# Kernel optimization log

Measured on AMD Instinct MI355X. Metric: run time of the kernel, lower is better.

The kernel has to match this reference:

```python
import jax, jax.numpy as jnp
import numpy as np

DIM = 512        # channels
QK = 512         # qk_dim (defaults to dim)
HEADS = 8
NWIN = 7         # windows per side
TOPK = 4
HD_QK = QK // HEADS
HD_V = DIM // HEADS


def setup_inputs() -> dict:
    key = jax.random.key(0)
    k0, k1, k2 = jax.random.split(key, 3)
    x = jax.random.normal(k0, (16, DIM, 56, 56), jnp.float32)
    w_qkv = jax.random.normal(k1, (2 * QK + DIM, DIM), jnp.float32) * 0.02
    b_qkv = jnp.zeros((2 * QK + DIM,), jnp.float32)
    w_lepe = jax.random.normal(k2, (DIM, 1, 3, 3), jnp.float32) * 0.02
    b_lepe = jnp.zeros((DIM,), jnp.float32)
    return {"x": x, "w_qkv": w_qkv, "b_qkv": b_qkv, "w_lepe": w_lepe, "b_lepe": b_lepe}


def _window(t, N, nwin, wh, ww):
    # (N, c, H, W) -> (N, p^2, w^2, c), matching 'n c (j h) (i w) -> n (j i) (h w) c'
    c = t.shape[1]
    t = t.reshape(N, c, nwin, wh, nwin, ww)
    return t.transpose(0, 2, 4, 3, 5, 1).reshape(N, nwin * nwin, wh * ww, c)


def reference(x, w_qkv, b_qkv, w_lepe, b_lepe):
    N, C, H, W = x.shape
    scale = QK ** -0.5
    wh, ww = H // NWIN, W // NWIN
    p2, w2 = NWIN * NWIN, wh * ww

    # QKVConv: 1x1 conv == per-pixel channel matmul
    qkv = jnp.einsum('nchw,oc->nohw', x, w_qkv) + b_qkv[None, :, None, None]
    q = qkv[:, :QK]          # (N, QK, H, W)
    kv = qkv[:, QK:]         # (N, QK+DIM, H, W)
    v = kv[:, QK:]           # (N, DIM, H, W)

    # lepe: depthwise 3x3 conv, stride 1 (stride_def==1 for dim=512/'small')
    lepe = jax.lax.conv_general_dilated(
        v, w_lepe, window_strides=(1, 1), padding='SAME',
        dimension_numbers=('NCHW', 'OIHW', 'NCHW'),
        feature_group_count=DIM) + b_lepe[None, :, None, None]

    q_pix = _window(q, N, NWIN, wh, ww)    # (N, p2, w2, QK)
    kv_pix = _window(kv, N, NWIN, wh, ww)  # (N, p2, w2, QK+DIM)

    # window-level routing queries/keys (detached: diff_routing=False)
    q_win = jax.lax.stop_gradient(q_pix.mean(axis=2))            # (N, p2, QK)
    k_win = jax.lax.stop_gradient(kv_pix[..., :QK].mean(axis=2))  # (N, p2, QK)

    # TopkRouting (emb is Identity since param_routing=False)
    attn_logit = jnp.einsum('npc,nmc->npm', q_win * scale, k_win)  # (N, p2, p2)
    topk_logit, r_idx = jax.lax.top_k(attn_logit, TOPK)            # (N, p2, TOPK)
    r_weight = jax.nn.softmax(topk_logit, axis=-1)                 # unused: mul_weight='none'

    # KVGather: kv_sel[n, p, t] = kv_pix[n, r_idx[n, p, t]]
    kv_sel = jax.vmap(lambda kvn, idxn: kvn[idxn])(kv_pix, r_idx)  # (N, p2, TOPK, w2, QK+DIM)

    k_sel = kv_sel[..., :QK].reshape(N, p2, TOPK * w2, HEADS, HD_QK)
    v_sel = kv_sel[..., QK:].reshape(N, p2, TOPK * w2, HEADS, HD_V)
    q_h = q_pix.reshape(N, p2, w2, HEADS, HD_QK)

    # per-window multi-head attention over gathered KV
    attn = jnp.einsum('npqhd,npkhd->nphqk', q_h * scale, k_sel)  # (N,p2,H,w2,TOPK*w2)
    attn = jax.nn.softmax(attn, axis=-1)
    out = jnp.einsum('nphqk,npkhd->npqhd', attn, v_sel)          # (N,p2,w2,HEADS,HD_V)
    out = out.reshape(N, NWIN, NWIN, wh, ww, DIM)
    out = out.transpose(0, 5, 1, 3, 2, 4).reshape(N, DIM, H, W)

    return out + lepe
```

## Files before the change

kernel.cpp:

```cpp
#include <hip/hip_runtime.h>

#define DEVI __device__ __forceinline__

typedef __attribute__((ext_vector_type(8))) short s16x8;
typedef __attribute__((ext_vector_type(4))) short s16x4;
typedef __attribute__((ext_vector_type(4))) float f32x4;

DEVI unsigned short f2b(float f) {
  union { float f; unsigned u; } v; v.f = f;
  return (unsigned short)((v.u + 0x7fffu + ((v.u >> 16) & 1u)) >> 16);
}
DEVI float b2f(unsigned short h) {
  union { unsigned u; float f; } v; v.u = ((unsigned)h) << 16;
  return v.f;
}

DEVI void gload16(const unsigned short* g, char* l) {
  __builtin_amdgcn_global_load_lds((const __attribute__((address_space(1))) void*)g,
                                   (__attribute__((address_space(3))) void*)l, 16, 0, 0);
}

__global__ __launch_bounds__(256) void k_transpose(const float* __restrict__ x,
                                                   unsigned short* __restrict__ xt,
                                                   float* __restrict__ rsum) {
  __shared__ unsigned short tile[64][68];
  __shared__ float ftile[64][65];
  const int s0 = blockIdx.x * 64, c0 = blockIdx.y * 64, n = blockIdx.z;
  const int t = threadIdx.x;
  const float* xp = x + (size_t)n * 512 * 3136;
  const int sl = t & 63;
  const int sg = s0 + sl;
#pragma unroll
  for (int pass = 0; pass < 4; ++pass) {
    const int quad = pass * 4 + (t >> 6);
    const int cc = quad * 4;
    unsigned short e[4];
#pragma unroll
    for (int jj = 0; jj < 4; ++jj) {
      float val = (sg < 3136) ? xp[(size_t)(c0 + cc + jj) * 3136 + sg] : 0.f;
      ftile[sl][cc + jj] = val;
      e[jj] = f2b(val);
    }
    s16x4 pk = {(short)e[0], (short)e[1], (short)e[2], (short)e[3]};
    *(s16x4*)(&tile[sl][cc]) = pk;
  }
  __syncthreads();
  unsigned short* xo = xt + ((size_t)n * 3200 + s0) * 512 + c0;
#pragma unroll
  for (int pass = 0; pass < 2; ++pass) {
    const int srow = pass * 32 + (t >> 3);
    const int ch = (t & 7) * 8;
    uint2 a = *(const uint2*)(&tile[srow][ch]);
    uint2 b = *(const uint2*)(&tile[srow][ch + 4]);
    uint4 val = {a.x, a.y, b.x, b.y};
    *(uint4*)(xo + (size_t)srow * 512 + ch) = val;
  }
  if (s0 < 3136) {
#pragma unroll
    for (int k = 0; k < 2; ++k) {
      const int idx = k * 256 + t;
      const int seg = idx >> 6, c = idx & 63;
      float s = 0.f;
#pragma unroll
      for (int e = 0; e < 8; ++e) s += ftile[seg * 8 + e][c];
      rsum[((size_t)n * 392 + (s0 >> 3) + seg) * 512 + c0 + c] = s;
    }
  }
}

__global__ __launch_bounds__(256) void k_wmean2(const float* __restrict__ rsum,
                                                float* __restrict__ xwm) {
  const int wi = blockIdx.x, n = blockIdx.y;
  const int wy = wi / 7, wx = wi % 7;
  const int t = threadIdx.x;
  float s0 = 0.f, s1 = 0.f;
#pragma unroll
  for (int dy = 0; dy < 8; ++dy) {
    const float* rp = rsum + ((size_t)n * 392 + (wy * 8 + dy) * 7 + wx) * 512;
    s0 += rp[t];
    s1 += rp[t + 256];
  }
  float* dst = xwm + ((size_t)n * 49 + wi) * 512;
  dst[t] = s0 * 0.015625f;
  dst[t + 256] = s1 * 0.015625f;
}

__global__ __launch_bounds__(256) void k_cvt_w(const float* __restrict__ w,
                                               unsigned short* __restrict__ wb) {
  const int i = (blockIdx.x * 256 + threadIdx.x) * 4;
  const float4 v = *(const float4*)(w + i);
  s16x4 pk = {(short)f2b(v.x), (short)f2b(v.y), (short)f2b(v.z), (short)f2b(v.w)};
  *(s16x4*)(wb + i) = pk;
}

__global__ __launch_bounds__(256) void k_qkv_gemm(
    const unsigned short* __restrict__ wb,
    const unsigned short* __restrict__ xt,
    const float* __restrict__ b_qkv,
    unsigned short* __restrict__ q_pix,
    unsigned short* __restrict__ k_pix,
    unsigned short* __restrict__ vwinT) {
  __shared__ char smem[34816];
  const int o0 = blockIdx.x * 128, s0 = blockIdx.y * 128, n = blockIdx.z;
  const int t = threadIdx.x;
  const int wave = t >> 6, lane = t & 63;
  const int wm = wave >> 1, wn = wave & 1;
  const int r15 = lane & 15, hi4 = lane >> 4;
  const unsigned short* Ag = wb + (size_t)o0 * 512;
  const unsigned short* Bg = xt + ((size_t)n * 3200 + s0) * 512;
  const int rch = lane >> 3;
  const int gsw = (lane & 7) ^ rch;

  f32x4 acc[4][4];
#pragma unroll
  for (int a = 0; a < 4; ++a)
#pragma unroll
    for (int b = 0; b < 4; ++b) acc[a][b] = (f32x4){0.f, 0.f, 0.f, 0.f};

  for (int kk = 0; kk < 8; ++kk) {
#pragma unroll
    for (int i = 0; i < 8; ++i) {
      const int chunk = i * 4 + wave;
      const unsigned short* base = (chunk < 16) ? Ag : Bg;
      const int row = (chunk & 15) * 8 + rch;
      gload16(base + (size_t)row * 512 + kk * 64 + gsw * 8, smem + (size_t)chunk * 1024);
    }
    __syncthreads();
    s16x8 af[2][4], bfr[2][4];
#pragma unroll
    for (int m = 0; m < 4; ++m) {
      const int ra = wm * 64 + m * 16 + r15;
      const int rb = wn * 64 + m * 16 + r15;
#pragma unroll
      for (int kb = 0; kb < 2; ++kb) {
        af[kb][m]  = *(const s16x8*)(smem + (size_t)ra * 128 + (((kb * 4 + hi4) ^ (ra & 7)) * 16));
        bfr[kb][m] = *(const s16x8*)(smem + 16384 + (size_t)rb * 128 + (((kb * 4 + hi4) ^ (rb & 7)) * 16));
      }
    }
#pragma unroll
    for (int kb = 0; kb < 2; ++kb)
#pragma unroll
      for (int m = 0; m < 4; ++m)
#pragma unroll
        for (int nf = 0; nf < 4; ++nf)
          acc[m][nf] = __builtin_amdgcn_mfma_f32_16x16x32_bf16(af[kb][m], bfr[kb][nf], acc[m][nf], 0, 0, 0);
    __syncthreads();
  }

  if (o0 >= 1024) {
    const int c0v = o0 - 1024;
    unsigned short* OT2 = (unsigned short*)smem;
#pragma unroll
    for (int m = 0; m < 4; ++m)
#pragma unroll
      for (int r = 0; r < 4; ++r) {
        const int ol = wm * 64 + m * 16 + hi4 * 4 + r;
        const float bia = b_qkv[o0 + ol];
#pragma unroll
        for (int nf = 0; nf < 4; ++nf) {
          const int sl = wn * 64 + nf * 16 + r15;
          OT2[(size_t)ol * 136 + sl] = f2b(acc[m][nf][r] + bia);
        }
      }
    __syncthreads();
#pragma unroll
    for (int i = 0; i < 8; ++i) {
      const int chunk = i * 256 + t;
      const int cl = chunk >> 4;
      const int sl = (chunk & 15) * 8;
      const int s = s0 + sl;
      if (s < 3136) {
        const uint4 val = *(const uint4*)(OT2 + (size_t)cl * 136 + sl);
        const int hh = s / 56, ww = s % 56;
        const int wdw = (hh >> 3) * 7 + (ww >> 3);
        const int key = (hh & 7) * 8;
        *(uint4*)(vwinT + (((size_t)n * 49 + wdw) * 512 + c0v + cl) * 64 + key) = val;
      }
    }
    return;
  }

  const bool isQ = (o0 < 512);
  const float sf = isQ ? 1.0f : 0.044194173824159216f;
  unsigned short* OT = (unsigned short*)smem;
#pragma unroll
  for (int m = 0; m < 4; ++m) {
    const int ol = wm * 64 + m * 16 + hi4 * 4;
    float bi_[4];
#pragma unroll
    for (int r = 0; r < 4; ++r) bi_[r] = b_qkv[o0 + ol + r];
#pragma unroll
    for (int nf = 0; nf < 4; ++nf) {
      const int sl = wn * 64 + nf * 16 + r15;
      s16x4 pk = {(short)f2b((acc[m][nf][0] + bi_[0]) * sf), (short)f2b((acc[m][nf][1] + bi_[1]) * sf),
                  (short)f2b((acc[m][nf][2] + bi_[2]) * sf), (short)f2b((acc[m][nf][3] + bi_[3]) * sf)};
      *(s16x4*)(OT + (size_t)sl * 132 + ol) = pk;
    }
  }
  __syncthreads();
#pragma unroll
  for (int pass = 0; pass < 8; ++pass) {
    const int sl = pass * 16 + (t >> 4);
    const int oh = (t & 15) * 8;
    const int s = s0 + sl;
    if (s < 3136) {
      const uint2 a = *(const uint2*)((char*)smem + (size_t)sl * 264 + oh * 2);
      const uint2 b = *(const uint2*)((char*)smem + (size_t)sl * 264 + oh * 2 + 8);
      const int hh = s / 56, ww = s % 56;
      const int wdw = (hh >> 3) * 7 + (ww >> 3);
      const int pi = (hh & 7) * 8 + (ww & 7);
      const int o = o0 + oh;
      const uint4 val = {a.x, a.y, b.x, b.y};
      if (isQ)
        *(uint4*)(q_pix + (((size_t)n * 49 + wdw) * 64 + pi) * 512 + o) = val;
      else
        *(uint4*)(k_pix + (((size_t)n * 49 + wdw) * 64 + pi) * 512 + (o - 512)) = val;
    }
  }
}

__global__ __launch_bounds__(256) void k_winproj(
    const float* __restrict__ xwm, const float* __restrict__ w_qkv,
    const float* __restrict__ b_qkv, float* __restrict__ qkw) {
  __shared__ float wss[64][65];
  __shared__ float xs[56][64];
  const int o0 = blockIdx.x * 64, n = blockIdx.y;
  const int t = threadIdx.x;
  const int ot = t & 31, pt = t >> 5;
  float acc0[7], acc1[7];
#pragma unroll
  for (int jj = 0; jj < 7; ++jj) { acc0[jj] = 0.f; acc1[jj] = 0.f; }
  for (int c0 = 0; c0 < 512; c0 += 64) {
    __syncthreads();
#pragma unroll
    for (int pass = 0; pass < 4; ++pass) {
      const int oo = (t >> 4) + pass * 16;
      const int cc = (t & 15) * 4;
      const float4 v = *(const float4*)(w_qkv + (size_t)(o0 + oo) * 512 + c0 + cc);
      wss[cc + 0][oo] = v.x; wss[cc + 1][oo] = v.y; wss[cc + 2][oo] = v.z; wss[cc + 3][oo] = v.w;
    }
#pragma unroll
    for (int i = 0; i < 14; ++i) {
      const int idx = i * 256 + t;
      const int p = idx >> 6, cc = idx & 63;
      xs[p][cc] = (p < 49) ? xwm[((size_t)n * 49 + p) * 512 + c0 + cc] : 0.f;
    }
    __syncthreads();
    for (int cc = 0; cc < 64; ++cc) {
      const float w0 = wss[cc][ot], w1 = wss[cc][ot + 32];
#pragma unroll
      for (int jj = 0; jj < 7; ++jj) {
        const float xv = xs[pt * 7 + jj][cc];
        acc0[jj] += w0 * xv;
        acc1[jj] += w1 * xv;
      }
    }
  }
#pragma unroll
  for (int jj = 0; jj < 7; ++jj) {
    const int p = pt * 7 + jj;
    if (p < 49) {
      float* dst = qkw + ((size_t)n * 49 + p) * 1024 + o0;
      dst[ot] = acc0[jj] + b_qkv[o0 + ot];
      dst[ot + 32] = acc1[jj] + b_qkv[o0 + ot + 32];
    }
  }
}

__global__ __launch_bounds__(256) void k_route(const float* __restrict__ qkw,
                                               int* __restrict__ ridx) {
  __shared__ float lg[49];
  const int bid = blockIdx.x, n = bid / 49, p = bid % 49;
  const int t = threadIdx.x, wave = t >> 6, lane = t & 63;
  const float* qr = qkw + (size_t)(n * 49 + p) * 1024 + lane * 8;
  const float4 qa = *(const float4*)qr;
  const float4 qb = *(const float4*)(qr + 4);
  for (int m = wave; m < 49; m += 4) {
    const float* kr = qkw + (size_t)(n * 49 + m) * 1024 + 512 + lane * 8;
    const float4 ka = *(const float4*)kr;
    const float4 kb = *(const float4*)(kr + 4);
    float s = qa.x * ka.x + qa.y * ka.y + qa.z * ka.z + qa.w * ka.w +
              qb.x * kb.x + qb.y * kb.y + qb.z * kb.z + qb.w * kb.w;
#pragma unroll
    for (int msk = 1; msk < 64; msk <<= 1) s += __shfl_xor(s, msk);
    if (lane == 0) lg[m] = s;
  }
  __syncthreads();
  if (t == 0) {
    float bv0 = -1e38f, bv1 = -1e38f, bv2 = -1e38f, bv3 = -1e38f;
    int bi0 = 0, bi1 = 0, bi2 = 0, bi3 = 0;
    for (int m = 0; m < 49; ++m) {
      const float v = lg[m];
      if (v > bv0) { bv3=bv2; bi3=bi2; bv2=bv1; bi2=bi1; bv1=bv0; bi1=bi0; bv0=v; bi0=m; }
      else if (v > bv1) { bv3=bv2; bi3=bi2; bv2=bv1; bi2=bi1; bv1=v; bi1=m; }
      else if (v > bv2) { bv3=bv2; bi3=bi2; bv2=v; bi2=m; }
      else if (v > bv3) { bv3=v; bi3=m; }
    }
    int4 w = {bi0, bi1, bi2, bi3};
    *(int4*)(ridx + bid * 4) = w;
  }
}

__global__ __launch_bounds__(256, 3) void k_attn(const unsigned short* __restrict__ q_pix,
                                                 const unsigned short* __restrict__ k_pix,
                                                 const unsigned short* __restrict__ vwinT,
                                                 const int* __restrict__ ridx,
                                                 unsigned short* __restrict__ owin) {
  __shared__ char smem[16384];
  const int bid = blockIdx.x;
  const int quad = bid & 3, nw = bid >> 2;
  const int n = nw / 49, wi = nw % 49;
  const int t = threadIdx.x;
  const int wv = t >> 6, lane = t & 63;
  const int task = quad * 4 + wv;
  const int h = task >> 1, half = task & 1;
  const int r15 = lane & 15, hi4 = lane >> 4;
  char* Pb = smem + wv * 4096;

  const unsigned short* Qb = q_pix + (((size_t)(n * 49 + wi) * 64) + half * 32) * 512 + h * 64;
  s16x8 qf[2][2];
#pragma unroll
  for (int qt = 0; qt < 2; ++qt)
#pragma unroll
    for (int kb = 0; kb < 2; ++kb)
      qf[qt][kb] = *(const s16x8*)(Qb + (size_t)(qt * 16 + r15) * 512 + kb * 32 + hi4 * 8);

  f32x4 oacc[2][4];
#pragma unroll
  for (int a = 0; a < 2; ++a)
#pragma unroll
    for (int b = 0; b < 4; ++b) oacc[a][b] = (f32x4){0.f, 0.f, 0.f, 0.f};
  float lrun[2];
#pragma unroll
  for (int a = 0; a < 2; ++a) lrun[a] = 0.f;

  const int4 rid = *(const int4*)(ridx + (n * 49 + wi) * 4);

  for (int j = 0; j < 4; ++j) {
    const int rw = (j == 0) ? rid.x : (j == 1) ? rid.y : (j == 2) ? rid.z : rid.w;
    const unsigned short* Kp = k_pix + ((size_t)(n * 49 + rw) * 64) * 512 + h * 64;
    const unsigned short* Vp = vwinT + ((size_t)(n * 49 + rw) * 512 + h * 64) * 64;

    s16x8 vc[8];
#pragma unroll
    for (int i = 0; i < 8; ++i) {
      const int kb = i >> 2, dt = i & 3;
      vc[i] = *(const s16x8*)(Vp + (size_t)(dt * 16 + r15) * 64 + kb * 32 + hi4 * 8);
    }

    f32x4 st[4][2];
#pragma unroll
    for (int a = 0; a < 4; ++a)
#pragma unroll
      for (int b = 0; b < 2; ++b) st[a][b] = (f32x4){0.f, 0.f, 0.f, 0.f};
#pragma unroll
    for (int kb = 0; kb < 2; ++kb) {
      s16x8 kf[4];
#pragma unroll
      for (int kt = 0; kt < 4; ++kt)
        kf[kt] = *(const s16x8*)(Kp + (size_t)(kt * 16 + r15) * 512 + kb * 32 + hi4 * 8);
#pragma unroll
      for (int kt = 0; kt < 4; ++kt)
#pragma unroll
        for (int qt = 0; qt < 2; ++qt)
          st[kt][qt] = __builtin_amdgcn_mfma_f32_16x16x32_bf16(kf[kt], qf[qt][kb], st[kt][qt], 0, 0, 0);
    }

#pragma unroll
    for (int qt = 0; qt < 2; ++qt) {
      float rs = 0.f;
#pragma unroll
      for (int kt = 0; kt < 4; ++kt)
#pragma unroll
        for (int r = 0; r < 4; ++r) {
          const float pv = __expf(st[kt][qt][r]);
          st[kt][qt][r] = pv;
          rs += pv;
        }
      lrun[qt] += rs;
    }

#pragma unroll
    for (int kt = 0; kt < 4; ++kt)
#pragma unroll
      for (int qt = 0; qt < 2; ++qt) {
        const int q = qt * 16 + r15;
#pragma unroll
        for (int rp = 0; rp < 4; rp += 2) {
          const int key = kt * 16 + hi4 * 4 + rp;
          const unsigned pk = (unsigned)f2b(st[kt][qt][rp]) | ((unsigned)f2b(st[kt][qt][rp + 1]) << 16);
          const int grp = (key >> 3) ^ (q & 7);
          *(unsigned*)(Pb + (size_t)q * 128 + grp * 16 + (key & 7) * 2) = pk;
        }
      }

#pragma unroll
    for (int kb = 0; kb < 2; ++kb) {
      s16x8 pf[2];
#pragma unroll
      for (int qm = 0; qm < 2; ++qm) {
        const int q = qm * 16 + r15;
        const int grp = (kb * 4 + hi4) ^ (q & 7);
        pf[qm] = *(const s16x8*)(Pb + (size_t)q * 128 + grp * 16);
      }
#pragma unroll
      for (int qm = 0; qm < 2; ++qm)
#pragma unroll
        for (int dt = 0; dt < 4; ++dt)
          oacc[qm][dt] = __builtin_amdgcn_mfma_f32_16x16x32_bf16(pf[qm], vc[kb * 4 + dt], oacc[qm][dt], 0, 0, 0);
    }
  }

#pragma unroll
  for (int qt = 0; qt < 2; ++qt) {
    lrun[qt] += __shfl_xor(lrun[qt], 16);
    lrun[qt] += __shfl_xor(lrun[qt], 32);
  }
#pragma unroll
  for (int qm = 0; qm < 2; ++qm)
#pragma unroll
    for (int r = 0; r < 4; ++r) {
      const float li = __shfl(lrun[qm], hi4 * 4 + r);
      const float inv = 1.0f / li;
#pragma unroll
      for (int dt = 0; dt < 4; ++dt) oacc[qm][dt][r] *= inv;
    }

#pragma unroll
  for (int qm = 0; qm < 2; ++qm)
#pragma unroll
    for (int dt = 0; dt < 4; ++dt) {
      const int d = dt * 16 + r15;
#pragma unroll
      for (int rp = 0; rp < 4; rp += 2) {
        const int q = qm * 16 + hi4 * 4 + rp;
        const unsigned pk = (unsigned)f2b(oacc[qm][dt][rp]) | ((unsigned)f2b(oacc[qm][dt][rp + 1]) << 16);
        const int chunk = (q >> 3) ^ (d & 3);
        *(unsigned*)(Pb + (size_t)d * 64 + chunk * 16 + (q & 7) * 2) = pk;
      }
    }

  unsigned short* ob = owin + (((size_t)(n * 49 + wi) * 512) + h * 64) * 64 + half * 32;
#pragma unroll
  for (int pass = 0; pass < 4; ++pass) {
    const int d = pass * 16 + (lane >> 2);
    const int qh = lane & 3;
    const int chunk = qh ^ (d & 3);
    const uint4 u = *(const uint4*)(Pb + (size_t)d * 64 + chunk * 16);
    *(uint4*)(ob + (size_t)d * 64 + qh * 8) = u;
  }
}

__global__ __launch_bounds__(256) void k_merge(const unsigned short* __restrict__ vwinT,
                                               const unsigned short* __restrict__ owin,
                                               const float* __restrict__ wl,
                                               const float* __restrict__ bl,
                                               float* __restrict__ out) {
  const int idx = blockIdx.x * 256 + threadIdx.x;
  const int chunk = idx % 392, c = (idx / 392) % 512, n = idx / (392 * 512);
  const int hr = chunk / 7, w0 = (chunk % 7) * 8;
  const int wx = w0 >> 3;
  const unsigned short* vb = vwinT + (size_t)n * 49 * 512 * 64;

  float rowv[3][10];
#pragma unroll
  for (int dy = 0; dy < 3; ++dy) {
    const int r = hr + dy - 1;
    if (r < 0 || r > 55) {
#pragma unroll
      for (int i = 0; i < 10; ++i) rowv[dy][i] = 0.f;
    } else {
      const int wb_ = (r >> 3) * 7, pr8 = (r & 7) * 8;
      const unsigned short* mid = vb + (((size_t)(wb_ + wx) * 512) + c) * 64 + pr8;
      const uint4 m = *(const uint4*)mid;
      const unsigned mm[4] = {m.x, m.y, m.z, m.w};
#pragma unroll
      for (int i = 0; i < 8; ++i)
        rowv[dy][i + 1] = b2f((unsigned short)((i & 1) ? (mm[i >> 1] >> 16) : (mm[i >> 1] & 0xffff)));
      rowv[dy][0] = (w0 > 0) ? b2f(vb[(((size_t)(wb_ + wx - 1) * 512) + c) * 64 + pr8 + 7]) : 0.f;
      rowv[dy][9] = (w0 < 48) ? b2f(vb[(((size_t)(wb_ + wx + 1) * 512) + c) * 64 + pr8]) : 0.f;
    }
  }

  float wv[9];
#pragma unroll
  for (int k = 0; k < 9; ++k) wv[k] = wl[c * 9 + k];
  const float bb = bl[c];

  float o[8];
#pragma unroll
  for (int jj = 0; jj < 8; ++jj) {
    float a = bb;
#pragma unroll
    for (int dy = 0; dy < 3; ++dy)
#pragma unroll
      for (int dx = 0; dx < 3; ++dx) a += rowv[dy][jj + dx] * wv[dy * 3 + dx];
    o[jj] = a;
  }

  const uint4 uo = *(const uint4*)(owin + (((size_t)(n * 49 + (hr >> 3) * 7 + wx) * 512) + c) * 64 + (hr & 7) * 8);
  const unsigned uu[4] = {uo.x, uo.y, uo.z, uo.w};
#pragma unroll
  for (int jj = 0; jj < 8; ++jj)
    o[jj] += b2f((unsigned short)((jj & 1) ? (uu[jj >> 1] >> 16) : (uu[jj >> 1] & 0xffff)));

  float* op = out + ((size_t)(n * 512 + c)) * 3136 + hr * 56 + w0;
  *(float4*)op = (float4){o[0], o[1], o[2], o[3]};
  *(float4*)(op + 4) = (float4){o[4], o[5], o[6], o[7]};
}

extern "C" void kernel_launch(void* const* d_in, const int* in_sizes, int n_in,
                              void* d_out, int out_size, void* d_ws, size_t ws_size,
                              hipStream_t stream) {
  const float* x = (const float*)d_in[0];
  const float* w_qkv = (const float*)d_in[1];
  const float* b_qkv = (const float*)d_in[2];
  const float* w_lepe = (const float*)d_in[3];
  const float* b_lepe = (const float*)d_in[4];
  float* out = (float*)d_out;

  char* ws = (char*)d_ws;
  size_t off = 0;
  auto alloc = [&](size_t bytes) {
    char* p = ws + off;
    off += (bytes + 255) & ~(size_t)255;
    return p;
  };
  unsigned short* xt     = (unsigned short*)alloc((size_t)16 * 3200 * 512 * 2);
  unsigned short* wb     = (unsigned short*)alloc((size_t)1536 * 512 * 2);
  unsigned short* q_pix  = (unsigned short*)alloc((size_t)16 * 49 * 64 * 512 * 2);
  unsigned short* k_pix  = (unsigned short*)alloc((size_t)16 * 49 * 64 * 512 * 2);
  unsigned short* vwinT  = (unsigned short*)alloc((size_t)16 * 49 * 512 * 64 * 2);
  unsigned short* owin   = (unsigned short*)alloc((size_t)16 * 49 * 512 * 64 * 2);
  float* rsum = (float*)alloc((size_t)16 * 392 * 512 * 4);
  float* xwm  = (float*)alloc((size_t)16 * 49 * 512 * 4);
  float* qkw  = (float*)alloc((size_t)16 * 49 * 1024 * 4);
  int* ridx   = (int*)alloc((size_t)16 * 49 * 4 * 4);

  k_transpose<<<dim3(50, 8, 16), 256, 0, stream>>>(x, xt, rsum);
  k_wmean2<<<dim3(49, 16), 256, 0, stream>>>(rsum, xwm);
  k_cvt_w<<<dim3(768), 256, 0, stream>>>(w_qkv, wb);
  k_qkv_gemm<<<dim3(12, 25, 16), 256, 0, stream>>>(wb, xt, b_qkv, q_pix, k_pix, vwinT);
  k_winproj<<<dim3(16, 16), 256, 0, stream>>>(xwm, w_qkv, b_qkv, qkw);
  k_route<<<dim3(784), 256, 0, stream>>>(qkw, ridx);
  k_attn<<<dim3(3136), 256, 0, stream>>>(q_pix, k_pix, vwinT, ridx, owin);
  k_merge<<<dim3(12544), 256, 0, stream>>>(vwinT, owin, w_lepe, b_lepe, out);
}
```

Before: 414.5 us.

## Use two waves per QKV GEMM block with 128x64 per-wave tiles

Reorganizes the QKV projection GEMM from four waves each computing a 64x64 tile to two waves each computing a 128x64 tile, with 128 threads per block. Each wave loads its B fragments once and reuses them across eight A row fragments, so fewer LDS reads are needed per MFMA. The trade-off is twice the accumulator registers per wave, fewer waves per block for hiding latency, and more global-to-LDS load and epilogue iterations per thread.

```diff
diff --git a/kernel.cpp b/kernel.cpp
--- a/kernel.cpp
+++ b/kernel.cpp
@@ -93,7 +93,7 @@
   *(s16x4*)(wb + i) = pk;
 }
 
-__global__ __launch_bounds__(256) void k_qkv_gemm(
+__global__ __launch_bounds__(128, 2) void k_qkv_gemm(
     const unsigned short* __restrict__ wb,
     const unsigned short* __restrict__ xt,
     const float* __restrict__ b_qkv,
@@ -104,46 +104,53 @@
   const int o0 = blockIdx.x * 128, s0 = blockIdx.y * 128, n = blockIdx.z;
   const int t = threadIdx.x;
   const int wave = t >> 6, lane = t & 63;
-  const int wm = wave >> 1, wn = wave & 1;
   const int r15 = lane & 15, hi4 = lane >> 4;
   const unsigned short* Ag = wb + (size_t)o0 * 512;
   const unsigned short* Bg = xt + ((size_t)n * 3200 + s0) * 512;
   const int rch = lane >> 3;
   const int gsw = (lane & 7) ^ rch;
 
-  f32x4 acc[4][4];
-#pragma unroll
-  for (int a = 0; a < 4; ++a)
+  f32x4 acc[8][4];
+#pragma unroll
+  for (int a = 0; a < 8; ++a)
 #pragma unroll
     for (int b = 0; b < 4; ++b) acc[a][b] = (f32x4){0.f, 0.f, 0.f, 0.f};
 
   for (int kk = 0; kk < 8; ++kk) {
 #pragma unroll
-    for (int i = 0; i < 8; ++i) {
-      const int chunk = i * 4 + wave;
+    for (int i = 0; i < 16; ++i) {
+      const int chunk = i * 2 + wave;
       const unsigned short* base = (chunk < 16) ? Ag : Bg;
       const int row = (chunk & 15) * 8 + rch;
       gload16(base + (size_t)row * 512 + kk * 64 + gsw * 8, smem + (size_t)chunk * 1024);
     }
     __syncthreads();
-    s16x8 af[2][4], bfr[2][4];
-#pragma unroll
-    for (int m = 0; m < 4; ++m) {
-      const int ra = wm * 64 + m * 16 + r15;
-      const int rb = wn * 64 + m * 16 + r15;
-#pragma unroll
-      for (int kb = 0; kb < 2; ++kb) {
-        af[kb][m]  = *(const s16x8*)(smem + (size_t)ra * 128 + (((kb * 4 + hi4) ^ (ra & 7)) * 16));
-        bfr[kb][m] = *(const s16x8*)(smem + 16384 + (size_t)rb * 128 + (((kb * 4 + hi4) ^ (rb & 7)) * 16));
-      }
-    }
-#pragma unroll
-    for (int kb = 0; kb < 2; ++kb)
-#pragma unroll
-      for (int m = 0; m < 4; ++m)
-#pragma unroll
-        for (int nf = 0; nf < 4; ++nf)
-          acc[m][nf] = __builtin_amdgcn_mfma_f32_16x16x32_bf16(af[kb][m], bfr[kb][nf], acc[m][nf], 0, 0, 0);
+    s16x8 bfr[2][4];
+#pragma unroll
+    for (int nf = 0; nf < 4; ++nf) {
+      const int rb = wave * 64 + nf * 16 + r15;
+#pragma unroll
+      for (int kb = 0; kb < 2; ++kb)
+        bfr[kb][nf] = *(const s16x8*)(smem + 16384 + (size_t)rb * 128 + (((kb * 4 + hi4) ^ (rb & 7)) * 16));
+    }
+#pragma unroll
+    for (int mh = 0; mh < 2; ++mh) {
+      s16x8 af[2][4];
+#pragma unroll
+      for (int m4 = 0; m4 < 4; ++m4) {
+        const int ra = (mh * 4 + m4) * 16 + r15;
+#pragma unroll
+        for (int kb = 0; kb < 2; ++kb)
+          af[kb][m4] = *(const s16x8*)(smem + (size_t)ra * 128 + (((kb * 4 + hi4) ^ (ra & 7)) * 16));
+      }
+#pragma unroll
+      for (int kb = 0; kb < 2; ++kb)
+#pragma unroll
+        for (int m4 = 0; m4 < 4; ++m4)
+#pragma unroll
+          for (int nf = 0; nf < 4; ++nf)
+            acc[mh * 4 + m4][nf] = __builtin_amdgcn_mfma_f32_16x16x32_bf16(af[kb][m4], bfr[kb][nf], acc[mh * 4 + m4][nf], 0, 0, 0);
+    }
     __syncthreads();
   }
 
@@ -151,21 +158,21 @@
     const int c0v = o0 - 1024;
     unsigned short* OT2 = (unsigned short*)smem;
 #pragma unroll
-    for (int m = 0; m < 4; ++m)
+    for (int m = 0; m < 8; ++m)
 #pragma unroll
       for (int r = 0; r < 4; ++r) {
-        const int ol = wm * 64 + m * 16 + hi4 * 4 + r;
+        const int ol = m * 16 + hi4 * 4 + r;
         const float bia = b_qkv[o0 + ol];
 #pragma unroll
         for (int nf = 0; nf < 4; ++nf) {
-          const int sl = wn * 64 + nf * 16 + r15;
+          const int sl = wave * 64 + nf * 16 + r15;
           OT2[(size_t)ol * 136 + sl] = f2b(acc[m][nf][r] + bia);
         }
       }
     __syncthreads();
 #pragma unroll
-    for (int i = 0; i < 8; ++i) {
-      const int chunk = i * 256 + t;
+    for (int i = 0; i < 16; ++i) {
+      const int chunk = i * 128 + t;
       const int cl = chunk >> 4;
       const int sl = (chunk & 15) * 8;
       const int s = s0 + sl;
@@ -184,14 +191,14 @@
   const float sf = isQ ? 1.0f : 0.044194173824159216f;
   unsigned short* OT = (unsigned short*)smem;
 #pragma unroll
-  for (int m = 0; m < 4; ++m) {
-    const int ol = wm * 64 + m * 16 + hi4 * 4;
+  for (int m = 0; m < 8; ++m) {
+    const int ol = m * 16 + hi4 * 4;
     float bi_[4];
 #pragma unroll
     for (int r = 0; r < 4; ++r) bi_[r] = b_qkv[o0 + ol + r];
 #pragma unroll
     for (int nf = 0; nf < 4; ++nf) {
-      const int sl = wn * 64 + nf * 16 + r15;
+      const int sl = wave * 64 + nf * 16 + r15;
       s16x4 pk = {(short)f2b((acc[m][nf][0] + bi_[0]) * sf), (short)f2b((acc[m][nf][1] + bi_[1]) * sf),
                   (short)f2b((acc[m][nf][2] + bi_[2]) * sf), (short)f2b((acc[m][nf][3] + bi_[3]) * sf)};
       *(s16x4*)(OT + (size_t)sl * 132 + ol) = pk;
@@ -199,8 +206,8 @@
   }
   __syncthreads();
 #pragma unroll
-  for (int pass = 0; pass < 8; ++pass) {
-    const int sl = pass * 16 + (t >> 4);
+  for (int pass = 0; pass < 16; ++pass) {
+    const int sl = pass * 8 + (t >> 4);
     const int oh = (t & 15) * 8;
     const int s = s0 + sl;
     if (s < 3136) {
@@ -540,7 +547,7 @@
   k_transpose<<<dim3(50, 8, 16), 256, 0, stream>>>(x, xt, rsum);
   k_wmean2<<<dim3(49, 16), 256, 0, stream>>>(rsum, xwm);
   k_cvt_w<<<dim3(768), 256, 0, stream>>>(w_qkv, wb);
-  k_qkv_gemm<<<dim3(12, 25, 16), 256, 0, stream>>>(wb, xt, b_qkv, q_pix, k_pix, vwinT);
+  k_qkv_gemm<<<dim3(12, 25, 16), 128, 0, stream>>>(wb, xt, b_qkv, q_pix, k_pix, vwinT);
   k_winproj<<<dim3(16, 16), 256, 0, stream>>>(xwm, w_qkv, b_qkv, qkw);
   k_route<<<dim3(784), 256, 0, stream>>>(qkw, ridx);
   k_attn<<<dim3(3136), 256, 0, stream>>>(q_pix, k_pix, vwinT, ridx, owin);
```

Result: no change. 410.7 us, median of 2 (-0.9%).
